# Optimization experiments

Hardware: AMD Instinct MI355X
Metric: run time of the kernel (lower is better)

The kernel has to match this reference:

```python
import jax, jax.numpy as jnp
import numpy as np

B, S = 16, 2048
VOCAB, N_KINGS = 32000, 27
D_EMB, D_MODEL = 256, 512
LN_EPS = 1e-5

def setup_inputs() -> dict:
    key = jax.random.key(0)
    ks = jax.random.split(key, 8)
    sequence = jax.random.randint(ks[0], (B, S), 0, VOCAB)
    king_id = jax.random.randint(ks[1], (B, 1), 0, N_KINGS)
    # stacked per-king token embedding tables (replaces dict-dispatched nn.Embedding modules)
    token_tables = jax.random.normal(ks[2], (N_KINGS, VOCAB, D_EMB), dtype=jnp.float32) * 0.02
    # nn.Bilinear(d_embedding, d_embedding, d_model): weight [M, E1, E2], bias [M]
    Wb = jax.random.normal(ks[3], (D_MODEL, D_EMB, D_EMB), dtype=jnp.float32) * (1.0 / np.sqrt(D_EMB))
    bb = jax.random.normal(ks[4], (D_MODEL,), dtype=jnp.float32) * 0.01
    king_table = jax.random.normal(ks[5], (N_KINGS, D_EMB), dtype=jnp.float32) * 0.02
    gamma = jnp.ones((D_MODEL,), dtype=jnp.float32)
    beta = jnp.zeros((D_MODEL,), dtype=jnp.float32)
    return {"sequence": sequence, "king_id": king_id, "token_tables": token_tables,
            "Wb": Wb, "bb": bb, "king_table": king_table, "gamma": gamma, "beta": beta}

def reference(sequence, king_id, token_tables, Wb, bb, king_table, gamma, beta):
    k = king_id[:, 0]                                  # [B]
    # batched dispatch: per-sample king-specific token embedding -> [B, S, E]
    tok = token_tables[k[:, None], sequence]
    kemb = king_table[k]                               # [B, E]
    # Bilinear(tok, kemb_repeated): kemb is constant over s, so contract it first.
    Wk = jnp.einsum('mij,bj->bmi', Wb, kemb)           # [B, M, E]
    x = jnp.einsum('bsi,bmi->bsm', tok, Wk) + bb       # [B, S, M]
    # LayerNorm over d_model
    mean = jnp.mean(x, axis=-1, keepdims=True)
    var = jnp.mean(jnp.square(x - mean), axis=-1, keepdims=True)
    return (x - mean) * jax.lax.rsqrt(var + LN_EPS) * gamma + beta
```

## Files before the change

### kernel.cpp

```cpp
#include <hip/hip_runtime.h>
#include <hip/hip_bf16.h>

#define B 16
#define S 2048
#define VOCAB 32000
#define D_EMB 256
#define D_MODEL 512
#define LN_EPS 1e-5f

using bf16x8 = __attribute__((ext_vector_type(8))) short;
using f32x4  = __attribute__((ext_vector_type(4))) float;

static __device__ __forceinline__ unsigned short f2bf(float f) {
    __hip_bfloat16 h = __float2bfloat16(f);
    return *reinterpret_cast<unsigned short*>(&h);
}

static __device__ __forceinline__ bf16x8 pack8(f32x4 v0, f32x4 v1) {
    union { unsigned short us[8]; bf16x8 v; } pk;
    pk.us[0] = f2bf(v0.x); pk.us[1] = f2bf(v0.y);
    pk.us[2] = f2bf(v0.z); pk.us[3] = f2bf(v0.w);
    pk.us[4] = f2bf(v1.x); pk.us[5] = f2bf(v1.y);
    pk.us[6] = f2bf(v1.z); pk.us[7] = f2bf(v1.w);
    return pk.v;
}

__global__ __launch_bounds__(256) void wk_mfma(
    const float* __restrict__ Wb,
    const float* __restrict__ king_table,
    const int* __restrict__ king_id,
    unsigned short* __restrict__ Wk)
{
    const int t    = threadIdx.x;
    const int lane = t & 63;
    const int wave = t >> 6;
    const int lr   = lane & 15;
    const int kg   = lane >> 4;

    const int kid = king_id[lr];
    const float* kp = king_table + (size_t)kid * D_EMB + kg * 8;
    bf16x8 bemb[8];
#pragma unroll
    for (int step = 0; step < 8; ++step) {
        f32x4 v0 = *(const f32x4*)(kp + step * 32);
        f32x4 v1 = *(const f32x4*)(kp + step * 32 + 4);
        bemb[step] = pack8(v0, v1);
    }

    const int rbase = (blockIdx.x * 4 + wave) * 64;

#pragma unroll
    for (int mf = 0; mf < 4; ++mf) {
        const float* arow = Wb + (size_t)(rbase + mf * 16 + lr) * D_EMB + kg * 8;
        f32x4 acc = {};
#pragma unroll
        for (int step = 0; step < 8; ++step) {
            f32x4 v0 = *(const f32x4*)(arow + step * 32);
            f32x4 v1 = *(const f32x4*)(arow + step * 32 + 4);
            acc = __builtin_amdgcn_mfma_f32_16x16x32_bf16(
                pack8(v0, v1), bemb[step], acc, 0, 0, 0);
        }
        union { unsigned short us[4]; uint2 q; } st;
        st.us[0] = f2bf(acc[0]); st.us[1] = f2bf(acc[1]);
        st.us[2] = f2bf(acc[2]); st.us[3] = f2bf(acc[3]);
        *(uint2*)(Wk + (size_t)lr * (D_MODEL * D_EMB) + rbase + mf * 16 + kg * 4) = st.q;
    }
}

#define TSB 64

__global__ __launch_bounds__(512, 4) void gemm_ln_mfma(
    const int* __restrict__ seq,
    const int* __restrict__ king_id,
    const float* __restrict__ token_tables,
    const unsigned short* __restrict__ Wk,
    const float* __restrict__ bb,
    const float* __restrict__ gamma,
    const float* __restrict__ beta,
    float* __restrict__ out)
{
    __shared__ unsigned short tokL[TSB][264];
    __shared__ float red_sum[8][TSB];
    __shared__ float red_sq[8][TSB];
    __shared__ float stats[2][TSB];

    const int b    = blockIdx.y;
    const int s0   = blockIdx.x * TSB;
    const int t    = threadIdx.x;
    const int lane = t & 63;
    const int wave = t >> 6;
    const int lr   = lane & 15;
    const int kg   = lane >> 4;

    const int kb = king_id[b];
    const float* ttab = token_tables + (size_t)kb * VOCAB * D_EMB;

    {
        int row = t >> 3;
        int ck  = (t & 7) * 32;
        int tokidx = seq[b * S + s0 + row];
        const float4* src = (const float4*)(ttab + (size_t)tokidx * D_EMB + ck);
#pragma unroll
        for (int u = 0; u < 4; ++u) {
            float4 v0 = src[u * 2 + 0];
            float4 v1 = src[u * 2 + 1];
            union { unsigned short us[8]; uint4 q; } pk;
            pk.us[0] = f2bf(v0.x); pk.us[1] = f2bf(v0.y);
            pk.us[2] = f2bf(v0.z); pk.us[3] = f2bf(v0.w);
            pk.us[4] = f2bf(v1.x); pk.us[5] = f2bf(v1.y);
            pk.us[6] = f2bf(v1.z); pk.us[7] = f2bf(v1.w);
            *(uint4*)&tokL[row][ck + u * 8] = pk.q;
        }
    }
    __syncthreads();

    const int m0 = wave * 64;
    const uint4* aptr[4];
    const uint4* bptr[4];
#pragma unroll
    for (int mf = 0; mf < 4; ++mf)
        aptr[mf] = (const uint4*)&tokL[mf * 16 + lr][kg * 8];
#pragma unroll
    for (int nf = 0; nf < 4; ++nf) {
        int col = m0 + nf * 16 + lr;
        bptr[nf] = (const uint4*)(Wk + ((size_t)(b * D_MODEL + col)) * D_EMB + kg * 8);
    }

    f32x4 acc[4][4] = {};

#pragma unroll
    for (int step = 0; step < 8; ++step) {
        bf16x8 af[4], bfr[4];
#pragma unroll
        for (int mf = 0; mf < 4; ++mf) {
            uint4 q = aptr[mf][step * 4];
            af[mf] = __builtin_bit_cast(bf16x8, q);
        }
#pragma unroll
        for (int nf = 0; nf < 4; ++nf) {
            uint4 q = bptr[nf][step * 4];
            bfr[nf] = __builtin_bit_cast(bf16x8, q);
        }
#pragma unroll
        for (int mf = 0; mf < 4; ++mf)
#pragma unroll
            for (int nf = 0; nf < 4; ++nf)
                acc[mf][nf] = __builtin_amdgcn_mfma_f32_16x16x32_bf16(
                    af[mf], bfr[nf], acc[mf][nf], 0, 0, 0);
    }

    float bbv[4], gv[4], bv[4];
#pragma unroll
    for (int nf = 0; nf < 4; ++nf) {
        int col = m0 + nf * 16 + lr;
        bbv[nf] = bb[col];
        gv[nf]  = gamma[col];
        bv[nf]  = beta[col];
    }

#pragma unroll
    for (int mf = 0; mf < 4; ++mf) {
#pragma unroll
        for (int r = 0; r < 4; ++r) {
            float sum = 0.0f, sq = 0.0f;
#pragma unroll
            for (int nf = 0; nf < 4; ++nf) {
                float v = acc[mf][nf][r] + bbv[nf];
                acc[mf][nf][r] = v;
                sum += v;
                sq  += v * v;
            }
#pragma unroll
            for (int off = 1; off < 16; off <<= 1) {
                sum += __shfl_xor(sum, off);
                sq  += __shfl_xor(sq, off);
            }
            if (lr == 0) {
                int row = mf * 16 + kg * 4 + r;
                red_sum[wave][row] = sum;
                red_sq[wave][row]  = sq;
            }
        }
    }
    __syncthreads();

    if (t < TSB) {
        float s = 0.0f, q = 0.0f;
#pragma unroll
        for (int w = 0; w < 8; ++w) { s += red_sum[w][t]; q += red_sq[w][t]; }
        float mean = s * (1.0f / D_MODEL);
        float var  = q * (1.0f / D_MODEL) - mean * mean;
        stats[0][t] = mean;
        stats[1][t] = rsqrtf(var + LN_EPS);
    }
    __syncthreads();

#pragma unroll
    for (int mf = 0; mf < 4; ++mf) {
#pragma unroll
        for (int r = 0; r < 4; ++r) {
            int row = mf * 16 + kg * 4 + r;
            float mean = stats[0][row];
            float rstd = stats[1][row];
            float* op = out + ((size_t)b * S + s0 + row) * D_MODEL + m0 + lr;
#pragma unroll
            for (int nf = 0; nf < 4; ++nf)
                op[nf * 16] = (acc[mf][nf][r] - mean) * rstd * gv[nf] + bv[nf];
        }
    }
}

extern "C" void kernel_launch(void* const* d_in, const int* in_sizes, int n_in,
                              void* d_out, int out_size, void* d_ws, size_t ws_size,
                              hipStream_t stream)
{
    const int*   seq          = (const int*)d_in[0];
    const int*   king_id      = (const int*)d_in[1];
    const float* token_tables = (const float*)d_in[2];
    const float* Wb           = (const float*)d_in[3];
    const float* bb           = (const float*)d_in[4];
    const float* king_table   = (const float*)d_in[5];
    const float* gamma        = (const float*)d_in[6];
    const float* beta         = (const float*)d_in[7];
    float* out = (float*)d_out;

    unsigned short* Wk = (unsigned short*)d_ws;

    wk_mfma<<<dim3((D_MODEL * D_EMB) / 256), dim3(256), 0, stream>>>(
        Wb, king_table, king_id, Wk);
    gemm_ln_mfma<<<dim3(S / TSB, B), dim3(512), 0, stream>>>(
        seq, king_id, token_tables, Wk, bb, gamma, beta, out);
}
```

Before: 63.27 us.

## Split token gather into two halves to overlap second-half loads with MFMA

The gather of token embeddings into shared memory is split along the embedding dimension. The first half is staged before the first barrier. The second-half global loads are issued into registers, the first four K-steps of MFMA run, and then the second half is packed into shared memory behind another barrier. The intent is to hide the gather latency of the second half behind compute, at the cost of an extra __syncthreads and more live registers.

```diff
diff --git a/kernel.cpp b/kernel.cpp
--- a/kernel.cpp
+++ b/kernel.cpp
@@ -95,24 +95,25 @@
     const int kb = king_id[b];
     const float* ttab = token_tables + (size_t)kb * VOCAB * D_EMB;
 
+    const int srow = t >> 3;
+    const int sck  = (t & 7) * 16;
+    const int tokidx = seq[b * S + s0 + srow];
+    const float* srcrow = ttab + (size_t)tokidx * D_EMB + sck;
+
     {
-        int row = t >> 3;
-        int ck  = (t & 7) * 32;
-        int tokidx = seq[b * S + s0 + row];
-        const float4* src = (const float4*)(ttab + (size_t)tokidx * D_EMB + ck);
-#pragma unroll
-        for (int u = 0; u < 4; ++u) {
-            float4 v0 = src[u * 2 + 0];
-            float4 v1 = src[u * 2 + 1];
-            union { unsigned short us[8]; uint4 q; } pk;
-            pk.us[0] = f2bf(v0.x); pk.us[1] = f2bf(v0.y);
-            pk.us[2] = f2bf(v0.z); pk.us[3] = f2bf(v0.w);
-            pk.us[4] = f2bf(v1.x); pk.us[5] = f2bf(v1.y);
-            pk.us[6] = f2bf(v1.z); pk.us[7] = f2bf(v1.w);
-            *(uint4*)&tokL[row][ck + u * 8] = pk.q;
-        }
-    }
-    __syncthreads();
+        f32x4 v0 = *(const f32x4*)(srcrow + 0);
+        f32x4 v1 = *(const f32x4*)(srcrow + 4);
+        f32x4 v2 = *(const f32x4*)(srcrow + 8);
+        f32x4 v3 = *(const f32x4*)(srcrow + 12);
+        *(bf16x8*)&tokL[srow][sck]     = pack8(v0, v1);
+        *(bf16x8*)&tokL[srow][sck + 8] = pack8(v2, v3);
+    }
+    __syncthreads();
+
+    f32x4 h0 = *(const f32x4*)(srcrow + 128);
+    f32x4 h1 = *(const f32x4*)(srcrow + 132);
+    f32x4 h2 = *(const f32x4*)(srcrow + 136);
+    f32x4 h3 = *(const f32x4*)(srcrow + 140);
 
     const int m0 = wave * 64;
     const uint4* aptr[4];
@@ -129,7 +130,32 @@
     f32x4 acc[4][4] = {};
 
 #pragma unroll
-    for (int step = 0; step < 8; ++step) {
+    for (int step = 0; step < 4; ++step) {
+        bf16x8 af[4], bfr[4];
+#pragma unroll
+        for (int mf = 0; mf < 4; ++mf) {
+            uint4 q = aptr[mf][step * 4];
+            af[mf] = __builtin_bit_cast(bf16x8, q);
+        }
+#pragma unroll
+        for (int nf = 0; nf < 4; ++nf) {
+            uint4 q = bptr[nf][step * 4];
+            bfr[nf] = __builtin_bit_cast(bf16x8, q);
+        }
+#pragma unroll
+        for (int mf = 0; mf < 4; ++mf)
+#pragma unroll
+            for (int nf = 0; nf < 4; ++nf)
+                acc[mf][nf] = __builtin_amdgcn_mfma_f32_16x16x32_bf16(
+                    af[mf], bfr[nf], acc[mf][nf], 0, 0, 0);
+    }
+
+    *(bf16x8*)&tokL[srow][128 + sck]     = pack8(h0, h1);
+    *(bf16x8*)&tokL[srow][128 + sck + 8] = pack8(h2, h3);
+    __syncthreads();
+
+#pragma unroll
+    for (int step = 4; step < 8; ++step) {
         bf16x8 af[4], bfr[4];
 #pragma unroll
         for (int mf = 0; mf < 4; ++mf) {
```

Result: faster. 60.00 us (-5.2%).
